# Optimization experiments

Hardware: AMD Instinct MI355X
Metric: run time of the kernel (lower is better)

## Reference

```python
import jax, jax.numpy as jnp
import numpy as np

DIM = 128
WS = 7
NUM_HEADS = 4
N = WS * WS
HEAD_DIM = DIM // NUM_HEADS
SCALE = HEAD_DIM ** (-0.5)


def _relative_position_index(ws):
    coords = np.stack(np.meshgrid(np.arange(ws), np.arange(ws), indexing='ij'))  # (2, ws, ws)
    cf = coords.reshape(2, -1)                      # (2, N)
    rel = cf[:, :, None] - cf[:, None, :]           # (2, N, N)
    rel = rel.transpose(1, 2, 0).astype(np.int64)   # (N, N, 2)
    rel[:, :, 0] += ws - 1
    rel[:, :, 1] += ws - 1
    rel[:, :, 0] *= 2 * ws - 1
    return rel.sum(-1)                              # (N, N) int


def setup_inputs() -> dict:
    key = jax.random.key(0)
    ks = jax.random.split(key, 8)
    B_ = 4096
    nW = 64
    x = jax.random.normal(ks[0], (B_, N, DIM), dtype=jnp.float32)
    mask = jax.random.normal(ks[1], (nW, N, N), dtype=jnp.float32)
    qkv_w = jax.random.normal(ks[2], (3 * DIM, DIM), dtype=jnp.float32) * 0.02
    qkv_b = jnp.zeros((3 * DIM,), dtype=jnp.float32)
    rpb_table = jax.random.normal(ks[3], ((2 * WS - 1) * (2 * WS - 1), NUM_HEADS), dtype=jnp.float32) * 0.02
    proj_w = jax.random.normal(ks[4], (DIM, DIM), dtype=jnp.float32) * 0.02
    proj_b = jnp.zeros((DIM,), dtype=jnp.float32)
    rel_index = jnp.asarray(_relative_position_index(WS), dtype=jnp.int32)
    return {"x": x, "mask": mask, "qkv_w": qkv_w, "qkv_b": qkv_b,
            "rpb_table": rpb_table, "proj_w": proj_w, "proj_b": proj_b,
            "rel_index": rel_index}


def reference(x, mask, qkv_w, qkv_b, rpb_table, proj_w, proj_b, rel_index):
    B_, n, C = x.shape
    H, hd = NUM_HEADS, HEAD_DIM
    qkv = x @ qkv_w.T + qkv_b                        # (B_, N, 3C)
    qkv = qkv.reshape(B_, n, 3, H, hd).transpose(2, 0, 3, 1, 4)  # (3, B_, H, N, hd)
    q, k, v = qkv[0] * SCALE, qkv[1], qkv[2]
    attn = jnp.einsum('bhnd,bhmd->bhnm', q, k)       # (B_, H, N, N)
    bias = rpb_table[rel_index.reshape(-1)].reshape(n, n, H).transpose(2, 0, 1)  # (H, N, N)
    attn = attn + bias[None]
    nW = mask.shape[0]
    attn = attn.reshape(B_ // nW, nW, H, n, n) + mask[None, :, None]
    attn = attn.reshape(B_, H, n, n)
    attn = jax.nn.softmax(attn, axis=-1)
    out = jnp.einsum('bhnm,bhmd->bnhd', attn, v).reshape(B_, n, C)
    return out @ proj_w.T + proj_b
```

## Files before the change

kernel.cpp:

```cpp
#include <hip/hip_runtime.h>
#include <hip/hip_bf16.h>
#include <stdint.h>

#define NTOK 49
#define DIMC 128
#define NHEAD 4
#define SCALE 0.17677669529663687f

typedef __bf16 bf16;
typedef __bf16 bf16x8 __attribute__((ext_vector_type(8)));
typedef __bf16 bf16x4 __attribute__((ext_vector_type(4)));
typedef float  f32x4  __attribute__((ext_vector_type(4)));
typedef short  s16x4  __attribute__((ext_vector_type(4)));

#define PW_OFF 0
#define K_OFF  16896
#define Q_OFF  26112
#define VT_OFF 35328
#define X0_OFF 44032
#define X1_OFF 52736
#define QK_S 36
#define VT_S 68
#define PW_S 132
#define X_S  136
#define SM_BYTES (61440 * 2)

#define WS_BIAS_OFF  524288
#define WS_QKVW_OFF  557056
#define WS_PROJW_OFF 655360

__device__ __forceinline__ f32x4 mfmaK32(bf16x8 a, bf16x8 b, f32x4 c) {
  return __builtin_amdgcn_mfma_f32_16x16x32_bf16(a, b, c, 0, 0, 0);
}
__device__ __forceinline__ f32x4 mfmaK16(bf16x4 a, bf16x4 b, f32x4 c) {
#if __has_builtin(__builtin_amdgcn_mfma_f32_16x16x16bf16_1k)
  return __builtin_amdgcn_mfma_f32_16x16x16bf16_1k(*(s16x4*)&a, *(s16x4*)&b, c,
                                                   0, 0, 0);
#else
  f32x4 d;
  asm("v_mfma_f32_16x16x16_bf16 %0, %1, %2, %3"
      : "=v"(d) : "v"(a), "v"(b), "v"(c));
  return d;
#endif
}
__device__ __forceinline__ bf16x8 cvt8p(f32x4 a, f32x4 c) {
  bf16x8 r;
#pragma unroll
  for (int j = 0; j < 4; ++j) { r[j] = (bf16)a[j]; r[4 + j] = (bf16)c[j]; }
  return r;
}
__device__ __forceinline__ void stage8(bf16* dst, const bf16* src) {
  bf16x8 v = *(const bf16x8*)src;
  bf16x4 lo, hi;
#pragma unroll
  for (int j = 0; j < 4; ++j) { lo[j] = v[j]; hi[j] = v[4 + j]; }
  *(bf16x4*)dst = lo;
  *(bf16x4*)(dst + 4) = hi;
}

__global__ __launch_bounds__(256)
void prep(const float* __restrict__ maskg, const float* __restrict__ rpb,
          const int* __restrict__ rel, const float* __restrict__ qkvw,
          const float* __restrict__ projw, bf16* __restrict__ mask_b,
          bf16* __restrict__ bias_b, bf16* __restrict__ qkvw_b,
          bf16* __restrict__ projw_b) {
  int id = blockIdx.x * 256 + threadIdx.x;
  if (id < 262144) {
    int c = id & 63, n = (id >> 6) & 63, win = id >> 12;
    int qd = c >> 4, mt = (c >> 2) & 3, r = c & 3;
    int m = mt * 16 + qd * 4 + r;
    float v = -30000.0f;
    if (n < NTOK && m < NTOK) v = maskg[((size_t)win * NTOK + n) * NTOK + m];
    mask_b[id] = (bf16)v;
  } else if (id < 262144 + 16384) {
    int t = id - 262144;
    int c = t & 63, h = (t >> 6) & 3, n = t >> 8;
    int qd = c >> 4, mt = (c >> 2) & 3, r = c & 3;
    int m = mt * 16 + qd * 4 + r;
    float v = 0.0f;
    if (n < NTOK && m < NTOK) v = rpb[rel[n * NTOK + m] * 4 + h];
    bias_b[t] = (bf16)v;
  } else if (id < 262144 + 16384 + 49152) {
    int t = id - (262144 + 16384);
    qkvw_b[t] = (bf16)qkvw[t];
  } else {
    int t = id - (262144 + 16384 + 49152);
    projw_b[t] = (bf16)projw[t];
  }
}

__global__ __launch_bounds__(512, 2)
void winattn(const float* __restrict__ xg, const float* __restrict__ qkvb,
             const float* __restrict__ projb, const bf16* __restrict__ mask_b,
             const bf16* __restrict__ bias_b, const bf16* __restrict__ qkvw_b,
             const bf16* __restrict__ projw_b, float* __restrict__ out) {
  extern __shared__ bf16 smd[];
  const int tid  = threadIdx.x;
  const int w8   = tid >> 6;
  const int lane = tid & 63;
  const int ln15 = lane & 15;
  const int quad = lane >> 4;
  const int h_kv = w8 >> 1, t_kv = w8 & 1;
  const int g2   = w8 & 3,  hp   = w8 >> 2;
  const int nq   = g2 * 16 + ln15;

  bf16* __restrict__ pwl = smd + PW_OFF;
  bf16* __restrict__ Kl  = smd + K_OFF;
  bf16* __restrict__ Ql  = smd + Q_OFF;
  bf16* __restrict__ VTl = smd + VT_OFF;

#pragma unroll
  for (int i = 0; i < 4; ++i) {
    int c = i * 512 + tid;
    int j = c >> 4, kc = (c & 15) * 8;
    stage8(&pwl[j * PW_S + kc], &projw_b[j * DIMC + kc]);
  }

  bf16x8 wqf[4], wkf[4], wvf[4];
#pragma unroll
  for (int ks = 0; ks < 4; ++ks) {
    wqf[ks] = *(const bf16x8*)&qkvw_b[(size_t)(          w8 * 16 + ln15) * DIMC + ks * 32 + quad * 8];
    wkf[ks] = *(const bf16x8*)&qkvw_b[(size_t)(DIMC    + w8 * 16 + ln15) * DIMC + ks * 32 + quad * 8];
    wvf[ks] = *(const bf16x8*)&qkvw_b[(size_t)(2 * DIMC + w8 * 16 + ln15) * DIMC + ks * 32 + quad * 8];
  }
  f32x4 qb = *(const f32x4*)&qkvb[w8 * 16 + quad * 4];
  f32x4 kb = *(const f32x4*)&qkvb[DIMC + w8 * 16 + quad * 4];
  float vb = qkvb[2 * DIMC + w8 * 16 + ln15];
  f32x4 pb[4];
#pragma unroll
  for (int j = 0; j < 4; ++j)
    pb[j] = *(const f32x4*)&projb[(hp * 4 + j) * 16 + quad * 4];
  bf16x4 bias4[2][4];
#pragma unroll
  for (int hh = 0; hh < 2; ++hh)
#pragma unroll
    for (int mt = 0; mt < 4; ++mt)
      bias4[hh][mt] = *(const bf16x4*)&bias_b[((nq * 4 + hp * 2 + hh) << 6) + quad * 16 + mt * 4];

  {
    const float* x0 = xg + (size_t)(blockIdx.x << 4) * (NTOK * DIMC);
    int r0 = w8 * 8 + quad, r1 = r0 + 4;
    const float* p0 = x0 + (r0 < NTOK ? r0 : NTOK - 1) * DIMC + ln15 * 8;
    const float* p1 = x0 + (r1 < NTOK ? r1 : NTOK - 1) * DIMC + ln15 * 8;
    f32x4 a0 = *(const f32x4*)p0, a1 = *(const f32x4*)(p0 + 4);
    f32x4 a2 = *(const f32x4*)p1, a3 = *(const f32x4*)(p1 + 4);
    *(bf16x8*)&smd[X0_OFF + r0 * X_S + ln15 * 8] = cvt8p(a0, a1);
    *(bf16x8*)&smd[X0_OFF + r1 * X_S + ln15 * 8] = cvt8p(a2, a3);
  }
  __syncthreads();

#pragma unroll 1
  for (int it = 0; it < 16; ++it) {
    const int b = (blockIdx.x << 4) + it;
    bf16* xc = smd + ((it & 1) ? X1_OFF : X0_OFF);
    bf16* xn = smd + ((it & 1) ? X0_OFF : X1_OFF);

    const int nit = it < 15 ? it + 1 : 15;
    const float* xnb = xg + (size_t)((blockIdx.x << 4) + nit) * (NTOK * DIMC);
    const int r0 = w8 * 8 + quad, r1 = r0 + 4;
    const float* np0 = xnb + (r0 < NTOK ? r0 : NTOK - 1) * DIMC + ln15 * 8;
    const float* np1 = xnb + (r1 < NTOK ? r1 : NTOK - 1) * DIMC + ln15 * 8;
    f32x4 nx0 = *(const f32x4*)np0, nx1 = *(const f32x4*)(np0 + 4);
    f32x4 nx2 = *(const f32x4*)np1, nx3 = *(const f32x4*)(np1 + 4);

    const bf16* mb = mask_b + (((size_t)(b & 63) * 64 + nq) << 6) + quad * 16;
    bf16x8 mk0 = *(const bf16x8*)mb;
    bf16x8 mk1 = *(const bf16x8*)(mb + 8);

#pragma unroll
    for (int g = 0; g < 4; ++g) {
      bf16x8 xf[4];
#pragma unroll
      for (int ks = 0; ks < 4; ++ks)
        xf[ks] = *(const bf16x8*)&xc[(g * 16 + ln15) * X_S + ks * 32 + quad * 8];
      f32x4 aq = (f32x4)(0.0f), ak = (f32x4)(0.0f), av = (f32x4)(0.0f);
#pragma unroll
      for (int ks = 0; ks < 4; ++ks) {
        aq = mfmaK32(wqf[ks], xf[ks], aq);
        ak = mfmaK32(wkf[ks], xf[ks], ak);
        av = mfmaK32(xf[ks], wvf[ks], av);
      }
      bf16x4 pq, pk, pv;
#pragma unroll
      for (int r = 0; r < 4; ++r) {
        pq[r] = (bf16)((aq[r] + qb[r]) * SCALE);
        pk[r] = (bf16)(ak[r] + kb[r]);
        pv[r] = (bf16)(av[r] + vb);
      }
      int rowqk = (h_kv * 64 + g * 16 + ln15) * QK_S + t_kv * 16 + quad * 4;
      *(bf16x4*)&Ql[rowqk] = pq;
      *(bf16x4*)&Kl[rowqk] = pk;
      *(bf16x4*)&VTl[(h_kv * 32 + t_kv * 16 + ln15) * VT_S + g * 16 + quad * 4] = pv;
    }
    __syncthreads();

    bf16* ob = xc;
#pragma unroll
    for (int hh = 0; hh < 2; ++hh) {
      const int h = hp * 2 + hh;
      bf16x4 qB0 = *(const bf16x4*)&Ql[(h * 64 + nq) * QK_S + quad * 4];
      bf16x4 qB1 = *(const bf16x4*)&Ql[(h * 64 + nq) * QK_S + 16 + quad * 4];
      f32x4 st[4];
#pragma unroll
      for (int mt = 0; mt < 4; ++mt) {
        const bf16* kr = &Kl[(h * 64 + mt * 16 + ln15) * QK_S + quad * 4];
        st[mt] = mfmaK16(*(const bf16x4*)(kr + 16), qB1,
                 mfmaK16(*(const bf16x4*)kr, qB0, (f32x4)(0.0f)));
      }
      float ssum = 0.0f;
      bf16x4 pw[4];
#pragma unroll
      for (int mt = 0; mt < 4; ++mt)
#pragma unroll
        for (int r = 0; r < 4; ++r) {
          float mv = (mt < 2) ? (float)mk0[mt * 4 + r] : (float)mk1[(mt - 2) * 4 + r];
          float v = fminf(st[mt][r] + mv + (float)bias4[hh][mt][r], 60.0f);
          float p = __expf(v);
          pw[mt][r] = (bf16)p;
          ssum += p;
        }
      ssum += __shfl_xor(ssum, 16);
      ssum += __shfl_xor(ssum, 32);
      f32x4 oa0 = (f32x4)(0.0f), oa1 = (f32x4)(0.0f);
#pragma unroll
      for (int mt = 0; mt < 4; ++mt) {
        oa0 = mfmaK16(*(const bf16x4*)&VTl[(h * 32 + ln15) * VT_S + mt * 16 + quad * 4], pw[mt], oa0);
        oa1 = mfmaK16(*(const bf16x4*)&VTl[(h * 32 + 16 + ln15) * VT_S + mt * 16 + quad * 4], pw[mt], oa1);
      }
      const float inv = 1.0f / ssum;
      bf16x4 o0, o1;
#pragma unroll
      for (int r = 0; r < 4; ++r) {
        o0[r] = (bf16)(oa0[r] * inv);
        o1[r] = (bf16)(oa1[r] * inv);
      }
      *(bf16x4*)&ob[nq * X_S + h * 32 + quad * 4] = o0;
      *(bf16x4*)&ob[nq * X_S + h * 32 + 16 + quad * 4] = o1;
    }

    *(bf16x8*)&xn[r0 * X_S + ln15 * 8] = cvt8p(nx0, nx1);
    *(bf16x8*)&xn[r1 * X_S + ln15 * 8] = cvt8p(nx2, nx3);
    __syncthreads();

    bf16x4 obf[8];
#pragma unroll
    for (int kt = 0; kt < 8; ++kt)
      obf[kt] = *(const bf16x4*)&ob[nq * X_S + kt * 16 + quad * 4];
    float* og = out + (size_t)b * (NTOK * DIMC) + nq * DIMC;
#pragma unroll
    for (int j = 0; j < 4; ++j) {
      const int jt = hp * 4 + j;
      f32x4 acc = (f32x4)(0.0f);
#pragma unroll
      for (int kt = 0; kt < 8; ++kt)
        acc = mfmaK16(*(const bf16x4*)&pwl[(jt * 16 + ln15) * PW_S + kt * 16 + quad * 4],
                      obf[kt], acc);
      if (nq < NTOK) {
        f32x4 y;
#pragma unroll
        for (int r = 0; r < 4; ++r) y[r] = acc[r] + pb[j][r];
        *(f32x4*)&og[jt * 16 + quad * 4] = y;
      }
    }
  }
}

extern "C" void kernel_launch(void* const* d_in, const int* in_sizes, int n_in,
                              void* d_out, int out_size, void* d_ws, size_t ws_size,
                              hipStream_t stream) {
  const float* x     = (const float*)d_in[0];
  const float* mask  = (const float*)d_in[1];
  const float* qkv_w = (const float*)d_in[2];
  const float* qkv_b = (const float*)d_in[3];
  const float* rpb   = (const float*)d_in[4];
  const float* prj_w = (const float*)d_in[5];
  const float* prj_b = (const float*)d_in[6];
  const int*   rel   = (const int*)d_in[7];
  float* out = (float*)d_out;

  bf16* ws_mask  = (bf16*)d_ws;
  bf16* ws_bias  = (bf16*)((char*)d_ws + WS_BIAS_OFF);
  bf16* ws_qkvw  = (bf16*)((char*)d_ws + WS_QKVW_OFF);
  bf16* ws_projw = (bf16*)((char*)d_ws + WS_PROJW_OFF);

  static int once = []() {
    hipFuncSetAttribute(reinterpret_cast<const void*>(winattn),
                        hipFuncAttributeMaxDynamicSharedMemorySize, SM_BYTES);
    return 0;
  }();
  (void)once;

  prep<<<1344, 256, 0, stream>>>(mask, rpb, rel, qkv_w, prj_w,
                                 ws_mask, ws_bias, ws_qkvw, ws_projw);
  winattn<<<256, 512, SM_BYTES, stream>>>(x, qkv_b, prj_b, ws_mask, ws_bias,
                                          ws_qkvw, ws_projw, out);
}
```

Baseline: 243.6 us.

## Shrink LDS with swizzled layouts, read proj weights from global, double grid

Replaces the padded LDS buffers with XOR-swizzled compact layouts and drops the double-buffered x tile and the LDS copy of the projection weights, which are now pre-permuted in the prep kernel and read straight from global memory. LDS drops to 64 KB, launch bounds rise to 4 waves per SIMD, and the grid doubles to 512 blocks of 8 windows each, aiming for higher occupancy and better latency hiding. QK^T and the projection now use K=32 MFMAs, and x, mask and output go through nontemporal loads and stores. In exchange there is an extra barrier per iteration, since the next x tile now overwrites the single buffer, and every wave reloads projection weights from global or L2.

```diff
diff --git a/kernel.cpp b/kernel.cpp
--- a/kernel.cpp
+++ b/kernel.cpp
@@ -13,21 +13,15 @@
 typedef float  f32x4  __attribute__((ext_vector_type(4)));
 typedef short  s16x4  __attribute__((ext_vector_type(4)));
 
-#define PW_OFF 0
-#define K_OFF  16896
-#define Q_OFF  26112
-#define VT_OFF 35328
-#define X0_OFF 44032
-#define X1_OFF 52736
-#define QK_S 36
-#define VT_S 68
-#define PW_S 132
-#define X_S  136
-#define SM_BYTES (61440 * 2)
+#define K_OFF  0
+#define QO_OFF 8192
+#define VT_OFF 16384
+#define X_OFF  24576
+#define SM_BYTES (32768 * 2)
 
 #define WS_BIAS_OFF  524288
 #define WS_QKVW_OFF  557056
-#define WS_PROJW_OFF 655360
+#define WS_PW_OFF    655360
 
 __device__ __forceinline__ f32x4 mfmaK32(bf16x8 a, bf16x8 b, f32x4 c) {
   return __builtin_amdgcn_mfma_f32_16x16x32_bf16(a, b, c, 0, 0, 0);
@@ -43,19 +37,15 @@
   return d;
 #endif
 }
+__device__ __forceinline__ int swz32(int row, int col)  { return row * 32  + (col ^ ((row & 3) << 3)); }
+__device__ __forceinline__ int swz64(int row, int col)  { return row * 64  + (col ^ ((row & 7) << 3)); }
+__device__ __forceinline__ int swz128(int row, int col) { return row * 128 + (col ^ ((row & 7) << 3)); }
+
 __device__ __forceinline__ bf16x8 cvt8p(f32x4 a, f32x4 c) {
   bf16x8 r;
 #pragma unroll
   for (int j = 0; j < 4; ++j) { r[j] = (bf16)a[j]; r[4 + j] = (bf16)c[j]; }
   return r;
-}
-__device__ __forceinline__ void stage8(bf16* dst, const bf16* src) {
-  bf16x8 v = *(const bf16x8*)src;
-  bf16x4 lo, hi;
-#pragma unroll
-  for (int j = 0; j < 4; ++j) { lo[j] = v[j]; hi[j] = v[4 + j]; }
-  *(bf16x4*)dst = lo;
-  *(bf16x4*)(dst + 4) = hi;
 }
 
 __global__ __launch_bounds__(256)
@@ -63,7 +53,7 @@
           const int* __restrict__ rel, const float* __restrict__ qkvw,
           const float* __restrict__ projw, bf16* __restrict__ mask_b,
           bf16* __restrict__ bias_b, bf16* __restrict__ qkvw_b,
-          bf16* __restrict__ projw_b) {
+          bf16* __restrict__ pw_b) {
   int id = blockIdx.x * 256 + threadIdx.x;
   if (id < 262144) {
     int c = id & 63, n = (id >> 6) & 63, win = id >> 12;
@@ -85,15 +75,18 @@
     qkvw_b[t] = (bf16)qkvw[t];
   } else {
     int t = id - (262144 + 16384 + 49152);
-    projw_b[t] = (bf16)projw[t];
-  }
-}
-
-__global__ __launch_bounds__(512, 2)
+    int j = t >> 7, k = t & 127;
+    int kb = k >> 5, u = k & 31;
+    int tt = u >> 4, q = (u >> 2) & 3, r = u & 3;
+    pw_b[j * 128 + kb * 32 + q * 8 + tt * 4 + r] = (bf16)projw[t];
+  }
+}
+
+__global__ __launch_bounds__(512, 4)
 void winattn(const float* __restrict__ xg, const float* __restrict__ qkvb,
              const float* __restrict__ projb, const bf16* __restrict__ mask_b,
              const bf16* __restrict__ bias_b, const bf16* __restrict__ qkvw_b,
-             const bf16* __restrict__ projw_b, float* __restrict__ out) {
+             const bf16* __restrict__ pw_b, float* __restrict__ out) {
   extern __shared__ bf16 smd[];
   const int tid  = threadIdx.x;
   const int w8   = tid >> 6;
@@ -104,32 +97,16 @@
   const int g2   = w8 & 3,  hp   = w8 >> 2;
   const int nq   = g2 * 16 + ln15;
 
-  bf16* __restrict__ pwl = smd + PW_OFF;
-  bf16* __restrict__ Kl  = smd + K_OFF;
-  bf16* __restrict__ Ql  = smd + Q_OFF;
-  bf16* __restrict__ VTl = smd + VT_OFF;
-
-#pragma unroll
-  for (int i = 0; i < 4; ++i) {
-    int c = i * 512 + tid;
-    int j = c >> 4, kc = (c & 15) * 8;
-    stage8(&pwl[j * PW_S + kc], &projw_b[j * DIMC + kc]);
-  }
-
   bf16x8 wqf[4], wkf[4], wvf[4];
 #pragma unroll
   for (int ks = 0; ks < 4; ++ks) {
-    wqf[ks] = *(const bf16x8*)&qkvw_b[(size_t)(          w8 * 16 + ln15) * DIMC + ks * 32 + quad * 8];
-    wkf[ks] = *(const bf16x8*)&qkvw_b[(size_t)(DIMC    + w8 * 16 + ln15) * DIMC + ks * 32 + quad * 8];
+    wqf[ks] = *(const bf16x8*)&qkvw_b[(size_t)(           w8 * 16 + ln15) * DIMC + ks * 32 + quad * 8];
+    wkf[ks] = *(const bf16x8*)&qkvw_b[(size_t)(DIMC     + w8 * 16 + ln15) * DIMC + ks * 32 + quad * 8];
     wvf[ks] = *(const bf16x8*)&qkvw_b[(size_t)(2 * DIMC + w8 * 16 + ln15) * DIMC + ks * 32 + quad * 8];
   }
   f32x4 qb = *(const f32x4*)&qkvb[w8 * 16 + quad * 4];
   f32x4 kb = *(const f32x4*)&qkvb[DIMC + w8 * 16 + quad * 4];
   float vb = qkvb[2 * DIMC + w8 * 16 + ln15];
-  f32x4 pb[4];
-#pragma unroll
-  for (int j = 0; j < 4; ++j)
-    pb[j] = *(const f32x4*)&projb[(hp * 4 + j) * 16 + quad * 4];
   bf16x4 bias4[2][4];
 #pragma unroll
   for (int hh = 0; hh < 2; ++hh)
@@ -137,42 +114,44 @@
     for (int mt = 0; mt < 4; ++mt)
       bias4[hh][mt] = *(const bf16x4*)&bias_b[((nq * 4 + hp * 2 + hh) << 6) + quad * 16 + mt * 4];
 
+  const int r0 = w8 * 8 + quad, r1 = r0 + 4;
+
   {
-    const float* x0 = xg + (size_t)(blockIdx.x << 4) * (NTOK * DIMC);
-    int r0 = w8 * 8 + quad, r1 = r0 + 4;
+    const float* x0 = xg + (size_t)(blockIdx.x << 3) * (NTOK * DIMC);
     const float* p0 = x0 + (r0 < NTOK ? r0 : NTOK - 1) * DIMC + ln15 * 8;
     const float* p1 = x0 + (r1 < NTOK ? r1 : NTOK - 1) * DIMC + ln15 * 8;
-    f32x4 a0 = *(const f32x4*)p0, a1 = *(const f32x4*)(p0 + 4);
-    f32x4 a2 = *(const f32x4*)p1, a3 = *(const f32x4*)(p1 + 4);
-    *(bf16x8*)&smd[X0_OFF + r0 * X_S + ln15 * 8] = cvt8p(a0, a1);
-    *(bf16x8*)&smd[X0_OFF + r1 * X_S + ln15 * 8] = cvt8p(a2, a3);
+    f32x4 a0 = __builtin_nontemporal_load((const f32x4*)p0);
+    f32x4 a1 = __builtin_nontemporal_load((const f32x4*)(p0 + 4));
+    f32x4 a2 = __builtin_nontemporal_load((const f32x4*)p1);
+    f32x4 a3 = __builtin_nontemporal_load((const f32x4*)(p1 + 4));
+    *(bf16x8*)&smd[X_OFF + swz128(r0, ln15 * 8)] = cvt8p(a0, a1);
+    *(bf16x8*)&smd[X_OFF + swz128(r1, ln15 * 8)] = cvt8p(a2, a3);
   }
   __syncthreads();
 
 #pragma unroll 1
-  for (int it = 0; it < 16; ++it) {
-    const int b = (blockIdx.x << 4) + it;
-    bf16* xc = smd + ((it & 1) ? X1_OFF : X0_OFF);
-    bf16* xn = smd + ((it & 1) ? X0_OFF : X1_OFF);
-
-    const int nit = it < 15 ? it + 1 : 15;
-    const float* xnb = xg + (size_t)((blockIdx.x << 4) + nit) * (NTOK * DIMC);
-    const int r0 = w8 * 8 + quad, r1 = r0 + 4;
+  for (int it = 0; it < 8; ++it) {
+    const int b = (blockIdx.x << 3) + it;
+
+    const int nit = it < 7 ? it + 1 : 7;
+    const float* xnb = xg + (size_t)((blockIdx.x << 3) + nit) * (NTOK * DIMC);
     const float* np0 = xnb + (r0 < NTOK ? r0 : NTOK - 1) * DIMC + ln15 * 8;
     const float* np1 = xnb + (r1 < NTOK ? r1 : NTOK - 1) * DIMC + ln15 * 8;
-    f32x4 nx0 = *(const f32x4*)np0, nx1 = *(const f32x4*)(np0 + 4);
-    f32x4 nx2 = *(const f32x4*)np1, nx3 = *(const f32x4*)(np1 + 4);
+    f32x4 nx0 = __builtin_nontemporal_load((const f32x4*)np0);
+    f32x4 nx1 = __builtin_nontemporal_load((const f32x4*)(np0 + 4));
+    f32x4 nx2 = __builtin_nontemporal_load((const f32x4*)np1);
+    f32x4 nx3 = __builtin_nontemporal_load((const f32x4*)(np1 + 4));
 
     const bf16* mb = mask_b + (((size_t)(b & 63) * 64 + nq) << 6) + quad * 16;
-    bf16x8 mk0 = *(const bf16x8*)mb;
-    bf16x8 mk1 = *(const bf16x8*)(mb + 8);
+    bf16x8 mk0 = __builtin_nontemporal_load((const bf16x8*)mb);
+    bf16x8 mk1 = __builtin_nontemporal_load((const bf16x8*)(mb + 8));
 
 #pragma unroll
     for (int g = 0; g < 4; ++g) {
       bf16x8 xf[4];
 #pragma unroll
       for (int ks = 0; ks < 4; ++ks)
-        xf[ks] = *(const bf16x8*)&xc[(g * 16 + ln15) * X_S + ks * 32 + quad * 8];
+        xf[ks] = *(const bf16x8*)&smd[X_OFF + swz128(g * 16 + ln15, ks * 32 + quad * 8)];
       f32x4 aq = (f32x4)(0.0f), ak = (f32x4)(0.0f), av = (f32x4)(0.0f);
 #pragma unroll
       for (int ks = 0; ks < 4; ++ks) {
@@ -187,25 +166,24 @@
         pk[r] = (bf16)(ak[r] + kb[r]);
         pv[r] = (bf16)(av[r] + vb);
       }
-      int rowqk = (h_kv * 64 + g * 16 + ln15) * QK_S + t_kv * 16 + quad * 4;
-      *(bf16x4*)&Ql[rowqk] = pq;
-      *(bf16x4*)&Kl[rowqk] = pk;
-      *(bf16x4*)&VTl[(h_kv * 32 + t_kv * 16 + ln15) * VT_S + g * 16 + quad * 4] = pv;
+      *(bf16x4*)&smd[QO_OFF + swz32(h_kv * 64 + g * 16 + ln15, t_kv * 16 + quad * 4)] = pq;
+      *(bf16x4*)&smd[K_OFF  + swz32(h_kv * 64 + g * 16 + ln15, t_kv * 16 + quad * 4)] = pk;
+      *(bf16x4*)&smd[VT_OFF + swz64(h_kv * 32 + t_kv * 16 + ln15, g * 16 + quad * 4)] = pv;
     }
     __syncthreads();
 
-    bf16* ob = xc;
+    *(bf16x8*)&smd[X_OFF + swz128(r0, ln15 * 8)] = cvt8p(nx0, nx1);
+    *(bf16x8*)&smd[X_OFF + swz128(r1, ln15 * 8)] = cvt8p(nx2, nx3);
+
 #pragma unroll
     for (int hh = 0; hh < 2; ++hh) {
       const int h = hp * 2 + hh;
-      bf16x4 qB0 = *(const bf16x4*)&Ql[(h * 64 + nq) * QK_S + quad * 4];
-      bf16x4 qB1 = *(const bf16x4*)&Ql[(h * 64 + nq) * QK_S + 16 + quad * 4];
+      bf16x8 qB = *(const bf16x8*)&smd[QO_OFF + swz32(h * 64 + nq, quad * 8)];
       f32x4 st[4];
 #pragma unroll
       for (int mt = 0; mt < 4; ++mt) {
-        const bf16* kr = &Kl[(h * 64 + mt * 16 + ln15) * QK_S + quad * 4];
-        st[mt] = mfmaK16(*(const bf16x4*)(kr + 16), qB1,
-                 mfmaK16(*(const bf16x4*)kr, qB0, (f32x4)(0.0f)));
+        bf16x8 k8 = *(const bf16x8*)&smd[K_OFF + swz32(h * 64 + mt * 16 + ln15, quad * 8)];
+        st[mt] = mfmaK32(k8, qB, (f32x4)(0.0f));
       }
       float ssum = 0.0f;
       bf16x4 pw[4];
@@ -224,44 +202,43 @@
       f32x4 oa0 = (f32x4)(0.0f), oa1 = (f32x4)(0.0f);
 #pragma unroll
       for (int mt = 0; mt < 4; ++mt) {
-        oa0 = mfmaK16(*(const bf16x4*)&VTl[(h * 32 + ln15) * VT_S + mt * 16 + quad * 4], pw[mt], oa0);
-        oa1 = mfmaK16(*(const bf16x4*)&VTl[(h * 32 + 16 + ln15) * VT_S + mt * 16 + quad * 4], pw[mt], oa1);
+        oa0 = mfmaK16(*(const bf16x4*)&smd[VT_OFF + swz64(h * 32 + ln15,      mt * 16 + quad * 4)], pw[mt], oa0);
+        oa1 = mfmaK16(*(const bf16x4*)&smd[VT_OFF + swz64(h * 32 + 16 + ln15, mt * 16 + quad * 4)], pw[mt], oa1);
       }
       const float inv = 1.0f / ssum;
-      bf16x4 o0, o1;
+      bf16x8 o8;
 #pragma unroll
       for (int r = 0; r < 4; ++r) {
-        o0[r] = (bf16)(oa0[r] * inv);
-        o1[r] = (bf16)(oa1[r] * inv);
-      }
-      *(bf16x4*)&ob[nq * X_S + h * 32 + quad * 4] = o0;
-      *(bf16x4*)&ob[nq * X_S + h * 32 + 16 + quad * 4] = o1;
+        o8[r]     = (bf16)(oa0[r] * inv);
+        o8[4 + r] = (bf16)(oa1[r] * inv);
+      }
+      *(bf16x8*)&smd[QO_OFF + swz32(h * 64 + nq, quad * 8)] = o8;
     }
-
-    *(bf16x8*)&xn[r0 * X_S + ln15 * 8] = cvt8p(nx0, nx1);
-    *(bf16x8*)&xn[r1 * X_S + ln15 * 8] = cvt8p(nx2, nx3);
     __syncthreads();
 
-    bf16x4 obf[8];
-#pragma unroll
-    for (int kt = 0; kt < 8; ++kt)
-      obf[kt] = *(const bf16x4*)&ob[nq * X_S + kt * 16 + quad * 4];
+    bf16x8 o8r[4];
+#pragma unroll
+    for (int kd = 0; kd < 4; ++kd)
+      o8r[kd] = *(const bf16x8*)&smd[QO_OFF + swz32(kd * 64 + nq, quad * 8)];
     float* og = out + (size_t)b * (NTOK * DIMC) + nq * DIMC;
 #pragma unroll
     for (int j = 0; j < 4; ++j) {
       const int jt = hp * 4 + j;
       f32x4 acc = (f32x4)(0.0f);
 #pragma unroll
-      for (int kt = 0; kt < 8; ++kt)
-        acc = mfmaK16(*(const bf16x4*)&pwl[(jt * 16 + ln15) * PW_S + kt * 16 + quad * 4],
-                      obf[kt], acc);
+      for (int kd = 0; kd < 4; ++kd) {
+        bf16x8 a8 = *(const bf16x8*)&pw_b[(size_t)(jt * 16 + ln15) * 128 + kd * 32 + quad * 8];
+        acc = mfmaK32(a8, o8r[kd], acc);
+      }
       if (nq < NTOK) {
+        f32x4 pbv = *(const f32x4*)&projb[jt * 16 + quad * 4];
         f32x4 y;
 #pragma unroll
-        for (int r = 0; r < 4; ++r) y[r] = acc[r] + pb[j][r];
-        *(f32x4*)&og[jt * 16 + quad * 4] = y;
+        for (int r = 0; r < 4; ++r) y[r] = acc[r] + pbv[r];
+        __builtin_nontemporal_store(y, (f32x4*)&og[jt * 16 + quad * 4]);
       }
     }
+    __syncthreads();
   }
 }
 
@@ -278,10 +255,10 @@
   const int*   rel   = (const int*)d_in[7];
   float* out = (float*)d_out;
 
-  bf16* ws_mask  = (bf16*)d_ws;
-  bf16* ws_bias  = (bf16*)((char*)d_ws + WS_BIAS_OFF);
-  bf16* ws_qkvw  = (bf16*)((char*)d_ws + WS_QKVW_OFF);
-  bf16* ws_projw = (bf16*)((char*)d_ws + WS_PROJW_OFF);
+  bf16* ws_mask = (bf16*)d_ws;
+  bf16* ws_bias = (bf16*)((char*)d_ws + WS_BIAS_OFF);
+  bf16* ws_qkvw = (bf16*)((char*)d_ws + WS_QKVW_OFF);
+  bf16* ws_pw   = (bf16*)((char*)d_ws + WS_PW_OFF);
 
   static int once = []() {
     hipFuncSetAttribute(reinterpret_cast<const void*>(winattn),
@@ -291,7 +268,7 @@
   (void)once;
 
   prep<<<1344, 256, 0, stream>>>(mask, rpb, rel, qkv_w, prj_w,
-                                 ws_mask, ws_bias, ws_qkvw, ws_projw);
-  winattn<<<256, 512, SM_BYTES, stream>>>(x, qkv_b, prj_b, ws_mask, ws_bias,
-                                          ws_qkvw, ws_projw, out);
-}
+                                 ws_mask, ws_bias, ws_qkvw, ws_pw);
+  winattn<<<512, 512, SM_BYTES, stream>>>(x, qkv_b, prj_b, ws_mask, ws_bias,
+                                          ws_qkvw, ws_pw, out);
+}
```

After: 428.9 us. 1.76x slower.
